# Optimization experiments

Measured on AMD Instinct MI355X. Metric: run time of the kernel, lower is better.

The kernel has to match this reference:

```python
import jax, jax.numpy as jnp
import numpy as np

N, H, T, G = 4096, 64, 6, 16  # nodes, hidden, topk kvecs, graphs


def _rope(h, pos, kvecs, batch):
    # h: [N,H], pos: [N,3], kvecs: [G,T,3], batch: [N]
    phase = jnp.einsum('nc,ntc->nt', pos, kvecs[batch])      # [N,T]
    cos = jnp.cos(phase).T[:, :, None]                        # [T,N,1]
    sin = jnp.sin(phase).T[:, :, None]
    a, b = h[:, 0::2], h[:, 1::2]                             # [N,H/2] each
    rot_a = a[None] * cos - b[None] * sin                     # [T,N,H/2]
    rot_b = a[None] * sin + b[None] * cos
    return jnp.concatenate([rot_a, rot_b], axis=-1)           # [T,N,H]


def setup_inputs() -> dict:
    key = jax.random.key(0)
    ks = jax.random.split(key, 8)
    node_feat = jax.random.normal(ks[0], (N, H), dtype=jnp.float32)
    node_feat_sr = jax.random.normal(ks[1], (N, H), dtype=jnp.float32)
    positions = jax.random.uniform(ks[2], (N, 3), dtype=jnp.float32) * 12.0  # ~bulk-water box
    kvecs = jax.random.normal(ks[3], (G, T, 3), dtype=jnp.float32)
    batch = jnp.sort(jax.random.randint(ks[4], (N,), 0, G)).astype(jnp.int32)
    W_readout = jax.random.normal(ks[5], (H, H), dtype=jnp.float32) / np.sqrt(H)
    W_qkv = jax.random.normal(ks[6], (3 * H, H), dtype=jnp.float32) / np.sqrt(H)
    W_tp = jax.random.normal(ks[7], (H, H, H), dtype=jnp.float32) / H
    return {'node_feat': node_feat, 'node_feat_sr': node_feat_sr,
            'positions': positions, 'kvecs': kvecs, 'batch': batch,
            'W_readout': W_readout, 'W_qkv': W_qkv, 'W_tp': W_tp}


def reference(node_feat, node_feat_sr, positions, kvecs, batch, W_readout, W_qkv, W_tp):
    scale_q = 1.0 / np.sqrt(H)
    scalars = node_feat @ W_readout.T                         # linear_readout -> [N,H]
    qkv = scalars @ W_qkv.T                                   # [N,3H]
    q, k, v = qkv[:, :H], qkv[:, H:2 * H], qkv[:, 2 * H:]
    q, k = jax.nn.silu(q), jax.nn.silu(k)
    q = _rope(q, positions, kvecs, batch) * scale_q           # [T,N,H]
    k = _rope(k, positions, kvecs, batch)                     # [T,N,H]
    # per-node outer product k (x) v, scatter-summed per graph
    kv_node = k[:, :, :, None] * v[None, :, None, :]          # [T,N,H,H]
    kv_graph = jax.ops.segment_sum(kv_node.transpose(1, 0, 2, 3), batch,
                                   num_segments=G)            # [G,T,H,H]
    # beta[t,n,e] = sum_d q[t,n,d] * kv_graph[batch[n],t,d,e]; update = beta.sum(0)
    update = jnp.einsum('tnd,ntde->ne', q, kv_graph[batch])   # [N,H]
    # FullyConnectedTensorProduct(Hx0e, Hx0e -> Hx0e) == bilinear form
    node_nl = jnp.einsum('ni,nj,kij->nk', node_feat_sr, update, W_tp)
    return node_nl
```

## Files before the change

### kernel.cpp

```cpp
#include <hip/hip_runtime.h>

#define N_NODES 4096
#define H 64
#define T_DIM 6
#define G_DIM 16

constexpr int OFF_W2   = 0;
constexpr int OFF_OFFS = 12288;
constexpr int OFF_QS   = 12320;
constexpr int OFF_KS   = OFF_QS + N_NODES * H;
constexpr int OFF_VS   = OFF_KS + N_NODES * H;
constexpr int OFF_COS  = OFF_VS + N_NODES * H;
constexpr int OFF_SIN  = OFF_COS + N_NODES * 8;
constexpr int OFF_KVG  = OFF_SIN + N_NODES * 8;
constexpr int OFF_UPD  = OFF_KVG + G_DIM * T_DIM * H * H;

typedef __bf16 bf16x8 __attribute__((ext_vector_type(8)));
typedef float f32x4 __attribute__((ext_vector_type(4)));

__global__ __launch_bounds__(256) void k_prep(const float* __restrict__ Wro,
                                              const float* __restrict__ Wqkv,
                                              const int* __restrict__ batch,
                                              float* __restrict__ ws) {
    int bid = blockIdx.x;
    if (bid < 48) {
        int o = bid * 256 + threadIdx.x;
        int i = o / 192, r = o % 192;
        float acc = 0.f;
        #pragma unroll 8
        for (int h = 0; h < 64; ++h) acc += Wqkv[r * 64 + h] * Wro[h * 64 + i];
        ws[OFF_W2 + i * 192 + r] = acc;
    } else {
        int g = threadIdx.x;
        if (g <= 16) {
            int lo = 0, hi = N_NODES;
            while (lo < hi) { int mid = (lo + hi) >> 1; if (batch[mid] < g) lo = mid + 1; else hi = mid; }
            ((int*)(ws + OFF_OFFS))[g] = lo;
        }
    }
}

__global__ __launch_bounds__(256) void k_qkv(const float* __restrict__ feat,
                                             const float* __restrict__ pos,
                                             const float* __restrict__ kvecs,
                                             const int* __restrict__ batch,
                                             float* __restrict__ ws) {
    __shared__ float Wl[12288];
    __shared__ float fl[16 * 64];
    int tid = threadIdx.x, blk = blockIdx.x;
    #pragma unroll
    for (int k = 0; k < 48; ++k) Wl[k * 256 + tid] = ws[OFF_W2 + k * 256 + tid];
    #pragma unroll
    for (int k = 0; k < 4; ++k) fl[k * 256 + tid] = feat[blk * 1024 + k * 256 + tid];
    __syncthreads();
    int w = tid >> 6, j = tid & 63;
    for (int mi = 0; mi < 4; ++mi) {
        int ml = w * 4 + mi;
        int n = blk * 16 + ml;
        float q = 0.f, kk = 0.f, v = 0.f;
        #pragma unroll 4
        for (int i = 0; i < 64; ++i) {
            float f = fl[ml * 64 + i];
            const float* wr = &Wl[i * 192];
            q += f * wr[j]; kk += f * wr[64 + j]; v += f * wr[128 + j];
        }
        float qs = q / (1.f + __expf(-q)) * 0.125f;
        float ks = kk / (1.f + __expf(-kk));
        ws[OFF_QS + n * 64 + j] = qs;
        ws[OFF_KS + n * 64 + j] = ks;
        ws[OFF_VS + n * 64 + j] = v;
        if (j < 6) {
            int g = batch[n];
            const float* kv = &kvecs[(g * 6 + j) * 3];
            float ph = pos[n * 3 + 0] * kv[0] + pos[n * 3 + 1] * kv[1] + pos[n * 3 + 2] * kv[2];
            ws[OFF_COS + n * 8 + j] = cosf(ph);
            ws[OFF_SIN + n * 8 + j] = sinf(ph);
        }
    }
}

__global__ __launch_bounds__(256) void k_kvg(float* __restrict__ ws) {
    __shared__ float kr8[8][64];
    __shared__ float v8[8][64];
    int bid = blockIdx.x;
    int g = bid / 48, rem = bid % 48, t = rem >> 3, ch = rem & 7;
    const int* off = (const int*)(ws + OFF_OFFS);
    int n0 = off[g] + ch * 64;
    int n1 = min(off[g + 1], n0 + 64);
    if (n0 >= n1) return;
    int tid = threadIdx.x;
    int e = tid & 63, dg = tid >> 6;
    float acc[16];
    #pragma unroll
    for (int k = 0; k < 16; ++k) acc[k] = 0.f;
    for (int base = n0; base < n1; base += 8) {
        int cnt = min(8, n1 - base);
        #pragma unroll
        for (int half = 0; half < 2; ++half) {
            int idx = half * 256 + tid;
            int ns = idx >> 6, d = idx & 63;
            float kr = 0.f, vv = 0.f;
            if (ns < cnt) {
                int n = base + ns;
                float ka = ws[OFF_KS + n * 64 + 2 * (d & 31)];
                float kb = ws[OFF_KS + n * 64 + 2 * (d & 31) + 1];
                float c = ws[OFF_COS + n * 8 + t], s = ws[OFF_SIN + n * 8 + t];
                kr = (d < 32) ? (ka * c - kb * s) : (ka * s + kb * c);
                vv = ws[OFF_VS + n * 64 + d];
            }
            kr8[ns][d] = kr; v8[ns][d] = vv;
        }
        __syncthreads();
        #pragma unroll
        for (int ns = 0; ns < 8; ++ns) {
            float vv = v8[ns][e];
            const float4* kp = (const float4*)&kr8[ns][dg * 16];
            #pragma unroll
            for (int q4 = 0; q4 < 4; ++q4) {
                float4 kq = kp[q4];
                acc[q4 * 4 + 0] += kq.x * vv; acc[q4 * 4 + 1] += kq.y * vv;
                acc[q4 * 4 + 2] += kq.z * vv; acc[q4 * 4 + 3] += kq.w * vv;
            }
        }
        __syncthreads();
    }
    float* kvg = ws + OFF_KVG + ((g * 6 + t) * 64 + dg * 16) * 64;
    #pragma unroll
    for (int k = 0; k < 16; ++k) atomicAdd(&kvg[k * 64 + e], acc[k]);
}

__global__ __launch_bounds__(256) void k_upd(const int* __restrict__ batch, float* __restrict__ ws) {
    __shared__ float qr[4][6][64];
    int tid = threadIdx.x, blk = blockIdx.x;
    #pragma unroll
    for (int k = 0; k < 6; ++k) {
        int idx = k * 256 + tid;
        int m = idx / 384, rem = idx % 384;
        int t = rem >> 6, d = rem & 63;
        int n = blk * 4 + m;
        float qa = ws[OFF_QS + n * 64 + 2 * (d & 31)];
        float qb = ws[OFF_QS + n * 64 + 2 * (d & 31) + 1];
        float c = ws[OFF_COS + n * 8 + t], s = ws[OFF_SIN + n * 8 + t];
        qr[m][t][d] = (d < 32) ? (qa * c - qb * s) : (qa * s + qb * c);
    }
    __syncthreads();
    int w = tid >> 6, e = tid & 63;
    int n = blk * 4 + w;
    int g = batch[n];
    const float* kvg = ws + OFF_KVG + g * (T_DIM * H * H);
    float acc = 0.f;
    #pragma unroll
    for (int t = 0; t < 6; ++t) {
        #pragma unroll 8
        for (int d = 0; d < 64; ++d)
            acc += qr[w][t][d] * kvg[(t * 64 + d) * 64 + e];
    }
    ws[OFF_UPD + n * 64 + e] = acc;
}

__device__ __forceinline__ bf16x8 make_afrag(const float* p, float s) {
    float4 u0 = *(const float4*)p;
    float4 u1 = *(const float4*)(p + 4);
    bf16x8 r;
    r[0] = (__bf16)(s * u0.x); r[1] = (__bf16)(s * u0.y); r[2] = (__bf16)(s * u0.z); r[3] = (__bf16)(s * u0.w);
    r[4] = (__bf16)(s * u1.x); r[5] = (__bf16)(s * u1.y); r[6] = (__bf16)(s * u1.z); r[7] = (__bf16)(s * u1.w);
    return r;
}
__device__ __forceinline__ bf16x8 make_bfrag(const float* p) {
    float4 u0 = *(const float4*)p;
    float4 u1 = *(const float4*)(p + 4);
    bf16x8 r;
    r[0] = (__bf16)u0.x; r[1] = (__bf16)u0.y; r[2] = (__bf16)u0.z; r[3] = (__bf16)u0.w;
    r[4] = (__bf16)u1.x; r[5] = (__bf16)u1.y; r[6] = (__bf16)u1.z; r[7] = (__bf16)u1.w;
    return r;
}

__global__ __launch_bounds__(256) void k_out(const float* __restrict__ sr,
                                             const float* __restrict__ Wtp,
                                             const float* __restrict__ ws,
                                             float* __restrict__ out) {
    __shared__ float sr_l[64][65];
    __shared__ float up_l[64][68];
    __shared__ float w_l[64][68];
    int tid = threadIdx.x;
    int mb = blockIdx.x & 63, kspl = blockIdx.x >> 6;
    int m0 = mb * 64;
    #pragma unroll
    for (int k = 0; k < 16; ++k) {
        int idx = k * 256 + tid;
        int m = idx >> 6, c = idx & 63;
        sr_l[m][c] = sr[(m0 + m) * 64 + c];
        up_l[m][c] = ws[OFF_UPD + (m0 + m) * 64 + c];
    }
    __syncthreads();
    int w = tid >> 6, lane = tid & 63;
    int wm = w >> 1, wn = w & 1;
    int lr = lane & 15, lg = lane >> 4;
    f32x4 acc[2][2];
    #pragma unroll
    for (int a = 0; a < 2; ++a)
        #pragma unroll
        for (int b = 0; b < 2; ++b) acc[a][b] = (f32x4){0.f, 0.f, 0.f, 0.f};

    for (int ii = 0; ii < 8; ++ii) {
        int i = kspl * 8 + ii;
        #pragma unroll
        for (int k = 0; k < 4; ++k) {
            int idx = k * 256 + tid;
            int col = idx >> 4, j4 = (idx & 15) * 4;
            float4 wv = *(const float4*)&Wtp[(col * 64 + i) * 64 + j4];
            *(float4*)&w_l[col][j4] = wv;
        }
        __syncthreads();
        float s0 = sr_l[wm * 32 + lr][i];
        float s1 = sr_l[wm * 32 + 16 + lr][i];
        #pragma unroll
        for (int kc = 0; kc < 2; ++kc) {
            int j0 = kc * 32 + lg * 8;
            bf16x8 a0 = make_afrag(&up_l[wm * 32 + lr][j0], s0);
            bf16x8 a1 = make_afrag(&up_l[wm * 32 + 16 + lr][j0], s1);
            bf16x8 b0 = make_bfrag(&w_l[wn * 32 + lr][j0]);
            bf16x8 b1 = make_bfrag(&w_l[wn * 32 + 16 + lr][j0]);
            acc[0][0] = __builtin_amdgcn_mfma_f32_16x16x32_bf16(a0, b0, acc[0][0], 0, 0, 0);
            acc[0][1] = __builtin_amdgcn_mfma_f32_16x16x32_bf16(a0, b1, acc[0][1], 0, 0, 0);
            acc[1][0] = __builtin_amdgcn_mfma_f32_16x16x32_bf16(a1, b0, acc[1][0], 0, 0, 0);
            acc[1][1] = __builtin_amdgcn_mfma_f32_16x16x32_bf16(a1, b1, acc[1][1], 0, 0, 0);
        }
        __syncthreads();
    }
    #pragma unroll
    for (int mt = 0; mt < 2; ++mt)
        #pragma unroll
        for (int nt = 0; nt < 2; ++nt) {
            int row = m0 + wm * 32 + mt * 16 + lg * 4;
            int col = wn * 32 + nt * 16 + lr;
            #pragma unroll
            for (int r = 0; r < 4; ++r)
                atomicAdd(&out[(row + r) * 64 + col], acc[mt][nt][r]);
        }
}

extern "C" void kernel_launch(void* const* d_in, const int* in_sizes, int n_in,
                              void* d_out, int out_size, void* d_ws, size_t ws_size,
                              hipStream_t stream) {
    const float* node_feat    = (const float*)d_in[0];
    const float* node_feat_sr = (const float*)d_in[1];
    const float* positions    = (const float*)d_in[2];
    const float* kvecs        = (const float*)d_in[3];
    const int*   batch        = (const int*)d_in[4];
    const float* W_readout    = (const float*)d_in[5];
    const float* W_qkv        = (const float*)d_in[6];
    const float* W_tp         = (const float*)d_in[7];
    float* out = (float*)d_out;
    float* ws  = (float*)d_ws;

    hipMemsetAsync(ws + OFF_KVG, 0, G_DIM * T_DIM * H * H * sizeof(float), stream);
    hipMemsetAsync(out, 0, N_NODES * H * sizeof(float), stream);

    k_prep<<<49, 256, 0, stream>>>(W_readout, W_qkv, batch, ws);
    k_qkv<<<256, 256, 0, stream>>>(node_feat, positions, kvecs, batch, ws);
    k_kvg<<<768, 256, 0, stream>>>(ws);
    k_upd<<<1024, 256, 0, stream>>>(batch, ws);
    k_out<<<512, 256, 0, stream>>>(node_feat_sr, W_tp, ws, out);
}
```

Measured before the change: 139.6 us.

## Fold prep and memsets into kernels, MFMA per-graph update

Removes the two memset launches and the k_prep kernel. The KV zeroing and graph-offset search move into k_qkv, and the output zeroing moves into k_upd. k_qkv no longer precomputes the fused weight: it does the two matmuls in sequence using padded shared memory and wave shuffles. k_upd is rewritten to tile nodes per graph and run bf16 MFMA against the per-graph kv tensor, applying rope on the fly. This cuts launch count and redundant kvg reads, at the cost of bf16 precision in the update and extra per-block matmul work.

```diff
diff --git a/kernel.cpp b/kernel.cpp
--- a/kernel.cpp
+++ b/kernel.cpp
@@ -1,71 +1,97 @@
 #include <hip/hip_runtime.h>
 
-#define N_NODES 4096
-#define H 64
-#define T_DIM 6
-#define G_DIM 16
-
-constexpr int OFF_W2   = 0;
-constexpr int OFF_OFFS = 12288;
-constexpr int OFF_QS   = 12320;
-constexpr int OFF_KS   = OFF_QS + N_NODES * H;
-constexpr int OFF_VS   = OFF_KS + N_NODES * H;
-constexpr int OFF_COS  = OFF_VS + N_NODES * H;
-constexpr int OFF_SIN  = OFF_COS + N_NODES * 8;
-constexpr int OFF_KVG  = OFF_SIN + N_NODES * 8;
-constexpr int OFF_UPD  = OFF_KVG + G_DIM * T_DIM * H * H;
+#define NN 4096
+#define HH 64
+#define TT 6
+#define GG 16
+
+constexpr int OFF_OFFS = 0;
+constexpr int OFF_QS   = 32;
+constexpr int OFF_KS   = OFF_QS + NN * HH;
+constexpr int OFF_VS   = OFF_KS + NN * HH;
+constexpr int OFF_COS  = OFF_VS + NN * HH;
+constexpr int OFF_SIN  = OFF_COS + NN * 8;
+constexpr int OFF_KVG  = OFF_SIN + NN * 8;
+constexpr int OFF_UPD  = OFF_KVG + GG * TT * HH * HH;
 
 typedef __bf16 bf16x8 __attribute__((ext_vector_type(8)));
 typedef float f32x4 __attribute__((ext_vector_type(4)));
-
-__global__ __launch_bounds__(256) void k_prep(const float* __restrict__ Wro,
-                                              const float* __restrict__ Wqkv,
-                                              const int* __restrict__ batch,
-                                              float* __restrict__ ws) {
-    int bid = blockIdx.x;
-    if (bid < 48) {
-        int o = bid * 256 + threadIdx.x;
-        int i = o / 192, r = o % 192;
-        float acc = 0.f;
-        #pragma unroll 8
-        for (int h = 0; h < 64; ++h) acc += Wqkv[r * 64 + h] * Wro[h * 64 + i];
-        ws[OFF_W2 + i * 192 + r] = acc;
-    } else {
-        int g = threadIdx.x;
-        if (g <= 16) {
-            int lo = 0, hi = N_NODES;
-            while (lo < hi) { int mid = (lo + hi) >> 1; if (batch[mid] < g) lo = mid + 1; else hi = mid; }
-            ((int*)(ws + OFF_OFFS))[g] = lo;
-        }
-    }
-}
 
 __global__ __launch_bounds__(256) void k_qkv(const float* __restrict__ feat,
                                              const float* __restrict__ pos,
                                              const float* __restrict__ kvecs,
                                              const int* __restrict__ batch,
+                                             const float* __restrict__ Wro,
+                                             const float* __restrict__ Wqkv,
                                              float* __restrict__ ws) {
-    __shared__ float Wl[12288];
-    __shared__ float fl[16 * 64];
     int tid = threadIdx.x, blk = blockIdx.x;
-    #pragma unroll
-    for (int k = 0; k < 48; ++k) Wl[k * 256 + tid] = ws[OFF_W2 + k * 256 + tid];
-    #pragma unroll
-    for (int k = 0; k < 4; ++k) fl[k * 256 + tid] = feat[blk * 1024 + k * 256 + tid];
+    if (blk == 256) {
+        int g = tid;
+        if (g <= GG) {
+            int lo = 0, hi = NN;
+            while (lo < hi) { int mid = (lo + hi) >> 1; if (batch[mid] < g) lo = mid + 1; else hi = mid; }
+            ((int*)(ws + OFF_OFFS))[g] = lo;
+        }
+        return;
+    }
+    {
+        float4 z = {0.f, 0.f, 0.f, 0.f};
+        float4* kz = (float4*)(ws + OFF_KVG) + blk * 384;
+        kz[tid] = z;
+        if (tid < 128) kz[256 + tid] = z;
+    }
+    __shared__ float Wro_l[64][66];
+    __shared__ float Wq_l[192][66];
+    #pragma unroll
+    for (int k = 0; k < 16; ++k) {
+        int idx = k * 256 + tid;
+        Wro_l[idx >> 6][idx & 63] = Wro[idx];
+    }
+    #pragma unroll
+    for (int k = 0; k < 48; ++k) {
+        int idx = k * 256 + tid;
+        Wq_l[idx >> 6][idx & 63] = Wqkv[idx];
+    }
     __syncthreads();
     int w = tid >> 6, j = tid & 63;
+    float fl[4];
+    #pragma unroll
+    for (int mi = 0; mi < 4; ++mi) fl[mi] = feat[(blk * 16 + w * 4 + mi) * 64 + j];
+    float scal[4] = {0.f, 0.f, 0.f, 0.f};
+    #pragma unroll
+    for (int i4 = 0; i4 < 16; ++i4) {
+        float4 w4 = *(const float4*)&Wro_l[j][i4 * 4];
+        #pragma unroll
+        for (int mi = 0; mi < 4; ++mi) {
+            scal[mi] += __shfl(fl[mi], i4 * 4 + 0, 64) * w4.x
+                      + __shfl(fl[mi], i4 * 4 + 1, 64) * w4.y
+                      + __shfl(fl[mi], i4 * 4 + 2, 64) * w4.z
+                      + __shfl(fl[mi], i4 * 4 + 3, 64) * w4.w;
+        }
+    }
+    float qa[4] = {0.f,0.f,0.f,0.f}, ka[4] = {0.f,0.f,0.f,0.f}, va[4] = {0.f,0.f,0.f,0.f};
+    #pragma unroll
+    for (int i4 = 0; i4 < 16; ++i4) {
+        float4 wq = *(const float4*)&Wq_l[j][i4 * 4];
+        float4 wk = *(const float4*)&Wq_l[64 + j][i4 * 4];
+        float4 wv = *(const float4*)&Wq_l[128 + j][i4 * 4];
+        #pragma unroll
+        for (int mi = 0; mi < 4; ++mi) {
+            float s0 = __shfl(scal[mi], i4 * 4 + 0, 64);
+            float s1 = __shfl(scal[mi], i4 * 4 + 1, 64);
+            float s2 = __shfl(scal[mi], i4 * 4 + 2, 64);
+            float s3 = __shfl(scal[mi], i4 * 4 + 3, 64);
+            qa[mi] += s0 * wq.x + s1 * wq.y + s2 * wq.z + s3 * wq.w;
+            ka[mi] += s0 * wk.x + s1 * wk.y + s2 * wk.z + s3 * wk.w;
+            va[mi] += s0 * wv.x + s1 * wv.y + s2 * wv.z + s3 * wv.w;
+        }
+    }
+    #pragma unroll
     for (int mi = 0; mi < 4; ++mi) {
-        int ml = w * 4 + mi;
-        int n = blk * 16 + ml;
-        float q = 0.f, kk = 0.f, v = 0.f;
-        #pragma unroll 4
-        for (int i = 0; i < 64; ++i) {
-            float f = fl[ml * 64 + i];
-            const float* wr = &Wl[i * 192];
-            q += f * wr[j]; kk += f * wr[64 + j]; v += f * wr[128 + j];
-        }
+        int n = blk * 16 + w * 4 + mi;
+        float q = qa[mi], kk2 = ka[mi], v = va[mi];
         float qs = q / (1.f + __expf(-q)) * 0.125f;
-        float ks = kk / (1.f + __expf(-kk));
+        float ks = kk2 / (1.f + __expf(-kk2));
         ws[OFF_QS + n * 64 + j] = qs;
         ws[OFF_KS + n * 64 + j] = ks;
         ws[OFF_VS + n * 64 + j] = v;
@@ -102,10 +128,10 @@
             float kr = 0.f, vv = 0.f;
             if (ns < cnt) {
                 int n = base + ns;
-                float ka = ws[OFF_KS + n * 64 + 2 * (d & 31)];
+                float ka2 = ws[OFF_KS + n * 64 + 2 * (d & 31)];
                 float kb = ws[OFF_KS + n * 64 + 2 * (d & 31) + 1];
                 float c = ws[OFF_COS + n * 8 + t], s = ws[OFF_SIN + n * 8 + t];
-                kr = (d < 32) ? (ka * c - kb * s) : (ka * s + kb * c);
+                kr = (d < 32) ? (ka2 * c - kb * s) : (ka2 * s + kb * c);
                 vv = ws[OFF_VS + n * 64 + d];
             }
             kr8[ns][d] = kr; v8[ns][d] = vv;
@@ -129,33 +155,60 @@
     for (int k = 0; k < 16; ++k) atomicAdd(&kvg[k * 64 + e], acc[k]);
 }
 
-__global__ __launch_bounds__(256) void k_upd(const int* __restrict__ batch, float* __restrict__ ws) {
-    __shared__ float qr[4][6][64];
-    int tid = threadIdx.x, blk = blockIdx.x;
-    #pragma unroll
-    for (int k = 0; k < 6; ++k) {
-        int idx = k * 256 + tid;
-        int m = idx / 384, rem = idx % 384;
-        int t = rem >> 6, d = rem & 63;
-        int n = blk * 4 + m;
-        float qa = ws[OFF_QS + n * 64 + 2 * (d & 31)];
-        float qb = ws[OFF_QS + n * 64 + 2 * (d & 31) + 1];
-        float c = ws[OFF_COS + n * 8 + t], s = ws[OFF_SIN + n * 8 + t];
-        qr[m][t][d] = (d < 32) ? (qa * c - qb * s) : (qa * s + qb * c);
-    }
-    __syncthreads();
-    int w = tid >> 6, e = tid & 63;
-    int n = blk * 4 + w;
-    int g = batch[n];
-    const float* kvg = ws + OFF_KVG + g * (T_DIM * H * H);
-    float acc = 0.f;
-    #pragma unroll
-    for (int t = 0; t < 6; ++t) {
-        #pragma unroll 8
-        for (int d = 0; d < 64; ++d)
-            acc += qr[w][t][d] * kvg[(t * 64 + d) * 64 + e];
-    }
-    ws[OFF_UPD + n * 64 + e] = acc;
+__global__ __launch_bounds__(256) void k_upd(float* __restrict__ ws, float* __restrict__ out) {
+    int tid = threadIdx.x, bid = blockIdx.x;
+    ((float4*)out)[bid * 256 + tid] = (float4){0.f, 0.f, 0.f, 0.f};
+    int g = bid >> 4, ch = bid & 15;
+    const int* off = (const int*)(ws + OFF_OFFS);
+    int n0 = off[g] + ch * 32;
+    int nend = off[g + 1];
+    if (n0 >= nend) return;
+    int w = tid >> 6, lane = tid & 63;
+    int wm = w & 1, wn = w >> 1;
+    int lr = lane & 15, lg = lane >> 4;
+    int nrow = n0 + wm * 16 + lr;
+    int nc = min(nrow, nend - 1);
+    float qv[16];
+    const float* qsr = ws + OFF_QS + nc * 64 + lg * 16;
+    #pragma unroll
+    for (int u = 0; u < 4; ++u) *(float4*)&qv[u * 4] = *(const float4*)&qsr[u * 4];
+    float cs[8], sn[8];
+    *(float4*)&cs[0] = *(const float4*)(ws + OFF_COS + nc * 8);
+    *(float4*)&cs[4] = *(const float4*)(ws + OFF_COS + nc * 8 + 4);
+    *(float4*)&sn[0] = *(const float4*)(ws + OFF_SIN + nc * 8);
+    *(float4*)&sn[4] = *(const float4*)(ws + OFF_SIN + nc * 8 + 4);
+    const float* kvg = ws + OFF_KVG + g * (TT * HH * HH);
+    int col0 = wn * 32 + lr, col1 = col0 + 16;
+    f32x4 acc0 = {0.f,0.f,0.f,0.f}, acc1 = {0.f,0.f,0.f,0.f};
+    #pragma unroll
+    for (int kk = 0; kk < 12; ++kk) {
+        int t = kk >> 1;
+        float c = cs[t], s = sn[t];
+        bf16x8 afr;
+        #pragma unroll
+        for (int ii = 0; ii < 8; ++ii) {
+            float a = qv[2 * ii], b = qv[2 * ii + 1];
+            float r = ((kk & 1) == 0) ? (a * c - b * s) : (a * s + b * c);
+            afr[ii] = (__bf16)r;
+        }
+        const float* bp = kvg + (kk * 32 + lg * 8) * 64;
+        bf16x8 b0, b1;
+        #pragma unroll
+        for (int i = 0; i < 8; ++i) {
+            b0[i] = (__bf16)bp[i * 64 + col0];
+            b1[i] = (__bf16)bp[i * 64 + col1];
+        }
+        acc0 = __builtin_amdgcn_mfma_f32_16x16x32_bf16(afr, b0, acc0, 0, 0, 0);
+        acc1 = __builtin_amdgcn_mfma_f32_16x16x32_bf16(afr, b1, acc1, 0, 0, 0);
+    }
+    #pragma unroll
+    for (int r = 0; r < 4; ++r) {
+        int n = n0 + wm * 16 + lg * 4 + r;
+        if (n < nend) {
+            ws[OFF_UPD + n * 64 + col0] = acc0[r];
+            ws[OFF_UPD + n * 64 + col1] = acc1[r];
+        }
+    }
 }
 
 __device__ __forceinline__ bf16x8 make_afrag(const float* p, float s) {
@@ -254,12 +307,8 @@
     float* out = (float*)d_out;
     float* ws  = (float*)d_ws;
 
-    hipMemsetAsync(ws + OFF_KVG, 0, G_DIM * T_DIM * H * H * sizeof(float), stream);
-    hipMemsetAsync(out, 0, N_NODES * H * sizeof(float), stream);
-
-    k_prep<<<49, 256, 0, stream>>>(W_readout, W_qkv, batch, ws);
-    k_qkv<<<256, 256, 0, stream>>>(node_feat, positions, kvecs, batch, ws);
+    k_qkv<<<257, 256, 0, stream>>>(node_feat, positions, kvecs, batch, W_readout, W_qkv, ws);
     k_kvg<<<768, 256, 0, stream>>>(ws);
-    k_upd<<<1024, 256, 0, stream>>>(batch, ws);
+    k_upd<<<256, 256, 0, stream>>>(ws, out);
     k_out<<<512, 256, 0, stream>>>(node_feat_sr, W_tp, ws, out);
 }
```

Measured after the change: 126.1 us. 9.6% less time.
